# Performance work log

Measured on AMD Instinct MI355X. Metric: run time of the kernel, lower is better.

Reference implementation:

```python
import jax, jax.numpy as jnp
import numpy as np

D_MODEL = 1024
NUM_HEADS = 16
D_K = D_MODEL // NUM_HEADS
R = 8
ALPHA = 16
SCALING = ALPHA / R


def _lora_linear(x, W, b, A, Bm):
    # base: x @ W.T + b ; lora: (x @ A.T) @ Bm.T * scaling
    base = jnp.einsum('btd,od->bto', x, W) + b
    lora = jnp.einsum('btr,or->bto', jnp.einsum('btd,rd->btr', x, A), Bm) * SCALING
    return base + lora


def setup_inputs() -> dict:
    key = jax.random.key(0)
    ks = jax.random.split(key, 20)
    B, T = 2, 2048
    inp = {
        'q': jax.random.normal(ks[0], (B, T, D_MODEL), jnp.float32),
        'k': jax.random.normal(ks[1], (B, T, D_MODEL), jnp.float32),
        'v': jax.random.normal(ks[2], (B, T, D_MODEL), jnp.float32),
        'mask': jnp.ones((1, 1, T, T), jnp.int32),
    }
    i = 3
    for name in ('q', 'k', 'v'):
        inp[f'W{name}'] = jax.random.normal(ks[i], (D_MODEL, D_MODEL), jnp.float32) * 0.02; i += 1
        inp[f'b{name}'] = jnp.zeros((D_MODEL,), jnp.float32)
        inp[f'A{name}'] = jax.random.normal(ks[i], (R, D_MODEL), jnp.float32) * 0.01; i += 1
        inp[f'B{name}'] = jax.random.normal(ks[i], (D_MODEL, R), jnp.float32) * 0.01; i += 1
    inp['Wo'] = jax.random.normal(ks[i], (D_MODEL, D_MODEL), jnp.float32) * 0.02
    inp['bo'] = jnp.zeros((D_MODEL,), jnp.float32)
    return inp


def reference(q, k, v, mask, Wq, bq, Aq, Bq, Wk, bk, Ak, Bk, Wv, bv, Av, Bv, Wo, bo):
    B, Tq, _ = q.shape
    Tk = k.shape[1]
    Q = _lora_linear(q, Wq, bq, Aq, Bq).reshape(B, Tq, NUM_HEADS, D_K).transpose(0, 2, 1, 3)
    K = _lora_linear(k, Wk, bk, Ak, Bk).reshape(B, Tk, NUM_HEADS, D_K).transpose(0, 2, 1, 3)
    V = _lora_linear(v, Wv, bv, Av, Bv).reshape(B, Tk, NUM_HEADS, D_K).transpose(0, 2, 1, 3)
    scores = jnp.einsum('bhqd,bhkd->bhqk', Q, K) / jnp.sqrt(jnp.float32(D_K))
    scores = jnp.where(mask == 0, jnp.float32(-1e9), scores)
    attn = jax.nn.softmax(scores, axis=-1)
    out = jnp.einsum('bhqk,bhkd->bhqd', attn, V)
    out = out.transpose(0, 2, 1, 3).reshape(B, Tq, D_MODEL)
    return jnp.einsum('btd,od->bto', out, Wo) + bo
```

## Files before the change

kernel.cpp:

```cpp
#include <hip/hip_runtime.h>
#include <stdint.h>

typedef unsigned short u16;
typedef __attribute__((ext_vector_type(4))) float f32x4;
typedef __attribute__((ext_vector_type(8))) __bf16 bf16x8;

#if __has_builtin(__builtin_amdgcn_exp2f)
#define EXP2(x) __builtin_amdgcn_exp2f(x)
#else
#define EXP2(x) exp2f(x)
#endif

static __device__ __forceinline__ float bf2f(u16 u) {
    union { uint32_t i; float f; } v; v.i = ((uint32_t)u) << 16; return v.f;
}
static __device__ __forceinline__ u16 f2bf(float f) {
    union { float f; uint32_t i; } v; v.f = f;
    return (u16)((v.i + 0x7FFFu + ((v.i >> 16) & 1u)) >> 16);
}

static __device__ __forceinline__ void gl2lds16(const u16* g, u16* lds) {
    __builtin_amdgcn_global_load_lds(
        (const __attribute__((address_space(1))) void*)g,
        (__attribute__((address_space(3))) void*)lds, 16, 0, 0);
}

struct CastArgs { const float* src[4]; u16* dst[4]; };

__global__ __launch_bounds__(256)
void cast_kernel(CastArgs a) {
    int bid = blockIdx.x;
    int arr = bid >> 6, boff = bid & 63;
    const float* s = a.src[arr] + (size_t)boff * 16384;
    u16* d = a.dst[arr] + (size_t)boff * 16384;
    const int tid = threadIdx.x;
#pragma unroll
    for (int i = 0; i < 8; ++i) {
        int c = tid + i * 256;
        float4 f0 = *(const float4*)(s + c * 8);
        float4 f1 = *(const float4*)(s + c * 8 + 4);
        u16 o[8];
        o[0] = f2bf(f0.x); o[1] = f2bf(f0.y); o[2] = f2bf(f0.z); o[3] = f2bf(f0.w);
        o[4] = f2bf(f1.x); o[5] = f2bf(f1.y); o[6] = f2bf(f1.z); o[7] = f2bf(f1.w);
        *(uint4*)(d + c * 8) = *(const uint4*)o;
    }
}

__global__ __launch_bounds__(256)
void flags_kernel(const int* __restrict__ mask, int* __restrict__ flags) {
    const int qb = blockIdx.x, kt = blockIdx.y;
    const int tid = threadIdx.x;
    int ok = 1;
#pragma unroll
    for (int i = 0; i < 8; ++i) {
        int c = tid + i * 256;
        int row = c >> 4, cg = c & 15;
        int4 m4 = *(const int4*)&mask[(size_t)(qb * 128 + row) * 2048 + kt * 64 + cg * 4];
        ok &= (m4.x != 0) & (m4.y != 0) & (m4.z != 0) & (m4.w != 0);
    }
    int wall = __all(ok) ? 1 : 0;
    __shared__ int red[4];
    if ((tid & 63) == 0) red[tid >> 6] = wall;
    __syncthreads();
    if (tid == 0) flags[qb * 32 + kt] = red[0] & red[1] & red[2] & red[3];
}

struct XaArgs { const float* x[3]; const float* A[3]; float* o[3]; u16* xb[3]; };

__global__ __launch_bounds__(256)
void xa_kernel(XaArgs a) {
    const int z = blockIdx.y;
    const int row = blockIdx.x * 4 + (threadIdx.x >> 6);
    const int lane = threadIdx.x & 63;
    const float* xr = a.x[z] + (size_t)row * 1024 + lane * 16;
    float xv[16];
#pragma unroll
    for (int j = 0; j < 4; ++j) *(float4*)&xv[j * 4] = *(const float4*)(xr + j * 4);
    {
        u16 ob[16];
#pragma unroll
        for (int j = 0; j < 16; ++j) ob[j] = f2bf(xv[j]);
        u16* dp = a.xb[z] + (size_t)row * 1024 + lane * 16;
        *(uint4*)dp = *(const uint4*)&ob[0];
        *(uint4*)(dp + 8) = *(const uint4*)&ob[8];
    }
    float s[8];
#pragma unroll
    for (int r = 0; r < 8; ++r) {
        const float* ar = a.A[z] + (size_t)r * 1024 + lane * 16;
        float av[16];
#pragma unroll
        for (int j = 0; j < 4; ++j) *(float4*)&av[j * 4] = *(const float4*)(ar + j * 4);
        float acc = 0.f;
#pragma unroll
        for (int j = 0; j < 16; ++j) acc += xv[j] * av[j];
#pragma unroll
        for (int off = 1; off < 64; off <<= 1) acc += __shfl_xor(acc, off, 64);
        s[r] = acc;
    }
    if (lane == 0) {
#pragma unroll
        for (int r = 0; r < 8; ++r) a.o[z][(size_t)row * 8 + r] = s[r];
    }
}

struct GemmPtrs { const u16* X; const u16* W; const float* bias; const float* XA; const float* Bm; void* out; int transT; float oscale; };
struct GemmArgs { GemmPtrs p[3]; };

#define LST 136
#define LTT 72

template <int WMT, int WNT, int LORA>
__global__ __launch_bounds__(256, 2)
void gemm_kernel(GemmArgs args) {
    constexpr int BM = WMT * 32, BN = WNT * 32;
    constexpr int MBLK = 4096 / BM;
    constexpr int IPA = BM / 32;
    constexpr int IPB = BN / 32;
    __shared__ alignas(16) u16 smem[(BM + BN) * 64];
    u16* As = smem;
    u16* Bs = smem + BM * 64;

    const GemmPtrs gp = args.p[blockIdx.z];
    const int tid = threadIdx.x;
    const int lane = tid & 63, wave = tid >> 6;
    const int wm = wave >> 1, wn = wave & 1;
    const int l15 = lane & 15, l4 = lane >> 4;
    const int id = blockIdx.x;
    const int m0 = (id % MBLK) * BM, n0 = (id / MBLK) * BN;

    const int srow = lane >> 3;
    const int scol = ((lane & 7) ^ srow) * 8;
    const u16* gA[IPA];
    const u16* gB[IPB];
#pragma unroll
    for (int i = 0; i < IPA; ++i) {
        int q = wave * IPA + i;
        gA[i] = gp.X + (size_t)(m0 + q * 8 + srow) * 1024 + scol;
    }
#pragma unroll
    for (int i = 0; i < IPB; ++i) {
        int q = wave * IPB + i;
        gB[i] = gp.W + (size_t)(n0 + q * 8 + srow) * 1024 + scol;
    }

    const f32x4 fz = {0.f, 0.f, 0.f, 0.f};
    f32x4 acc[WMT][WNT];
#pragma unroll
    for (int i = 0; i < WMT; ++i)
#pragma unroll
        for (int j = 0; j < WNT; ++j) acc[i][j] = fz;

    const int sw = l15 & 7;
    for (int kb = 0; kb < 16; ++kb) {
        __syncthreads();
#pragma unroll
        for (int i = 0; i < IPA; ++i)
            gl2lds16(gA[i] + kb * 64, &As[(wave * IPA + i) * 512]);
#pragma unroll
        for (int i = 0; i < IPB; ++i)
            gl2lds16(gB[i] + kb * 64, &Bs[(wave * IPB + i) * 512]);
        __syncthreads();
#pragma unroll
        for (int kk2 = 0; kk2 < 2; ++kk2) {
            bf16x8 af[WMT], bfr[WNT];
#pragma unroll
            for (int mt = 0; mt < WMT; ++mt) {
                int x = wm * (WMT * 16) + mt * 16 + l15;
                af[mt] = *(const bf16x8*)&As[x * 64 + (((kk2 * 4 + l4) ^ sw) * 8)];
            }
#pragma unroll
            for (int nt = 0; nt < WNT; ++nt) {
                int y = wn * (WNT * 16) + nt * 16 + l15;
                bfr[nt] = *(const bf16x8*)&Bs[y * 64 + (((kk2 * 4 + l4) ^ sw) * 8)];
            }
#pragma unroll
            for (int mt = 0; mt < WMT; ++mt)
#pragma unroll
                for (int nt = 0; nt < WNT; ++nt)
                    acc[mt][nt] = __builtin_amdgcn_mfma_f32_16x16x32_bf16(af[mt], bfr[nt], acc[mt][nt], 0, 0, 0);
        }
    }

    if constexpr (LORA) {
        __syncthreads();
        float* XAs = (float*)smem;
        float* Bms = (float*)(smem + BM * 64);
        {
            int rr = tid >> 1, hf = (tid & 1) * 4;
            *(float4*)&XAs[rr * 8 + hf] = *(const float4*)&gp.XA[(size_t)(m0 + rr) * 8 + hf];
            if (tid < 128) {
                *(float4*)&Bms[tid * 8]     = *(const float4*)&gp.Bm[(size_t)(n0 + tid) * 8];
                *(float4*)&Bms[tid * 8 + 4] = *(const float4*)&gp.Bm[(size_t)(n0 + tid) * 8 + 4];
            }
        }
        __syncthreads();
        const float osc = gp.oscale;
        float bmv[WNT][8], bsv[WNT];
#pragma unroll
        for (int nt = 0; nt < WNT; ++nt) {
            int nloc = wn * 64 + nt * 16 + l15;
            bsv[nt] = gp.bias[n0 + nloc];
#pragma unroll
            for (int q8 = 0; q8 < 8; ++q8) bmv[nt][q8] = Bms[nloc * 8 + q8];
        }
#pragma unroll
        for (int mt = 0; mt < WMT; ++mt)
#pragma unroll
            for (int r = 0; r < 4; ++r) {
                int mloc = wm * 64 + mt * 16 + l4 * 4 + r;
                float xa8[8];
                *(float4*)&xa8[0] = *(const float4*)&XAs[mloc * 8];
                *(float4*)&xa8[4] = *(const float4*)&XAs[mloc * 8 + 4];
#pragma unroll
                for (int nt = 0; nt < WNT; ++nt) {
                    float lora = 0.f;
#pragma unroll
                    for (int q8 = 0; q8 < 8; ++q8) lora += xa8[q8] * bmv[nt][q8];
                    acc[mt][nt][r] = (acc[mt][nt][r] + bsv[nt] + 2.0f * lora) * osc;
                }
            }
        __syncthreads();

        u16* outp = (u16*)gp.out;
        const int bb = m0 >> 11;
        if (gp.transT) {
            u16* Lst = smem;
#pragma unroll
            for (int ch = 0; ch < 2; ++ch) {
#pragma unroll
                for (int mt2 = 0; mt2 < 2; ++mt2) {
                    int mt = ch * 2 + mt2;
#pragma unroll
                    for (int nt = 0; nt < WNT; ++nt)
#pragma unroll
                        for (int r = 0; r < 4; ++r)
                            Lst[(wn * 64 + nt * 16 + l15) * LTT + wm * 32 + mt2 * 16 + l4 * 4 + r] =
                                f2bf(acc[mt][nt][r]);
                }
                __syncthreads();
#pragma unroll
                for (int j = 0; j < 4; ++j) {
                    int w = tid + j * 256;
                    int nl = w >> 3, seg = w & 7;
                    uint4 val = *(const uint4*)&Lst[nl * LTT + seg * 8];
                    int n = n0 + nl, hh = n >> 6, dd = n & 63;
                    int c0 = seg * 8;
                    int gm = m0 + (c0 >> 5) * 64 + ch * 32 + (c0 & 31);
                    int t = gm & 2047;
                    *(uint4*)&outp[(((size_t)(bb * 16 + hh)) * 64 + dd) * 2048 + t] = val;
                }
                __syncthreads();
            }
        } else {
            u16* Ls = smem;
#pragma unroll
            for (int ch = 0; ch < 2; ++ch) {
#pragma unroll
                for (int mt2 = 0; mt2 < 2; ++mt2) {
                    int mt = ch * 2 + mt2;
#pragma unroll
                    for (int nt = 0; nt < WNT; ++nt)
#pragma unroll
                        for (int r = 0; r < 4; ++r)
                            Ls[(wm * 32 + mt2 * 16 + l4 * 4 + r) * LST + wn * 64 + nt * 16 + l15] =
                                f2bf(acc[mt][nt][r]);
                }
                __syncthreads();
#pragma unroll
                for (int j = 0; j < 4; ++j) {
                    int w = tid + j * 256;
                    int lrow = w >> 4, seg = w & 15;
                    uint4 val = *(const uint4*)&Ls[lrow * LST + seg * 8];
                    int gm = m0 + (lrow >> 5) * 64 + ch * 32 + (lrow & 31);
                    int t = gm & 2047;
                    int n = n0 + seg * 8, hh = n >> 6, dd = n & 63;
                    *(uint4*)&outp[(((size_t)(bb * 16 + hh)) * 2048 + t) * 64 + dd] = val;
                }
                __syncthreads();
            }
        }
    } else {
        float* outp = (float*)gp.out;
#pragma unroll
        for (int mt = 0; mt < WMT; ++mt)
#pragma unroll
            for (int r = 0; r < 4; ++r) {
                int m = m0 + wm * (WMT * 16) + mt * 16 + l4 * 4 + r;
#pragma unroll
                for (int nt = 0; nt < WNT; ++nt) {
                    int n = n0 + wn * (WNT * 16) + nt * 16 + l15;
                    outp[(size_t)m * 1024 + n] = acc[mt][nt][r] + gp.bias[n];
                }
            }
    }
}

#define EXP2C (-5.7707801636f)

__global__ __launch_bounds__(256, 4)
void attn_kernel(const u16* __restrict__ QKV, const int* __restrict__ mask,
                 const int* __restrict__ flags, u16* __restrict__ Xo) {
    const int qb = blockIdx.x >> 5;
    const int bh = blockIdx.x & 31;
    const int b = bh >> 4, h = bh & 15;
    const int tid = threadIdx.x;
    const int lane = tid & 63, wave = tid >> 6;
    const int l15 = lane & 15, l4 = lane >> 4;

    __shared__ alignas(16) u16 Ks[2][64 * 64];
    __shared__ alignas(16) u16 Vts[2][64 * 64];
    __shared__ alignas(16) u16 Ps[64 * 64];

    const size_t plane = (size_t)2 * 16 * 2048 * 64;
    const u16* Qg = QKV + (size_t)(b * 16 + h) * 2048 * 64;
    const u16* Kg = Qg + plane;
    const u16* Vg = Kg + plane;

    const int srow = lane >> 3;
    const int scol = ((lane & 7) ^ srow) * 8;

    bf16x8 qa[2];
#pragma unroll
    for (int kk2 = 0; kk2 < 2; ++kk2)
        qa[kk2] = *(const bf16x8*)&Qg[(size_t)(qb * 64 + wave * 16 + l15) * 64 + kk2 * 32 + l4 * 8];

    const f32x4 fz = {0.f, 0.f, 0.f, 0.f};
    f32x4 accO[4];
    float lsum[4];
#pragma unroll
    for (int dt = 0; dt < 4; ++dt) accO[dt] = fz;
#pragma unroll
    for (int r = 0; r < 4; ++r) lsum[r] = 0.f;

#pragma unroll
    for (int i = 0; i < 2; ++i) {
        int qq = wave * 2 + i;
        gl2lds16(Kg + (size_t)(qq * 8 + srow) * 64 + scol, &Ks[0][qq * 512]);
        gl2lds16(Vg + (size_t)(qq * 8 + srow) * 2048 + scol, &Vts[0][qq * 512]);
    }
    __syncthreads();

    for (int kt = 0; kt < 32; ++kt) {
        const u16* Kc = &Ks[kt & 1][0];
        const u16* Vc = &Vts[kt & 1][0];

        if (kt < 31) {
            u16* Kn = &Ks[(kt + 1) & 1][0];
            u16* Vn = &Vts[(kt + 1) & 1][0];
#pragma unroll
            for (int i = 0; i < 2; ++i) {
                int qq = wave * 2 + i;
                gl2lds16(Kg + (size_t)((kt + 1) * 64 + qq * 8 + srow) * 64 + scol, &Kn[qq * 512]);
                gl2lds16(Vg + (size_t)(qq * 8 + srow) * 2048 + (kt + 1) * 64 + scol, &Vn[qq * 512]);
            }
        }

        f32x4 accS[4];
#pragma unroll
        for (int nt = 0; nt < 4; ++nt) accS[nt] = fz;
#pragma unroll
        for (int kk2 = 0; kk2 < 2; ++kk2) {
            bf16x8 kf[4];
#pragma unroll
            for (int nt = 0; nt < 4; ++nt)
                kf[nt] = *(const bf16x8*)&Kc[(nt * 16 + l15) * 64 + (((kk2 * 4 + l4) ^ (l15 & 7)) * 8)];
#pragma unroll
            for (int nt = 0; nt < 4; ++nt)
                accS[nt] = __builtin_amdgcn_mfma_f32_16x16x32_bf16(qa[kk2], kf[nt], accS[nt], 0, 0, 0);
        }

        if (flags[(qb >> 1) * 32 + kt] == 0) {
#pragma unroll
            for (int nt = 0; nt < 4; ++nt)
#pragma unroll
                for (int r = 0; r < 4; ++r) {
                    int qrow = qb * 64 + wave * 16 + l4 * 4 + r;
                    int kcol = kt * 64 + nt * 16 + l15;
                    if (mask[(size_t)qrow * 2048 + kcol] == 0) accS[nt][r] = -1e9f;
                }
        }

#pragma unroll
        for (int r = 0; r < 4; ++r) {
            float part = 0.f;
#pragma unroll
            for (int nt = 0; nt < 4; ++nt) {
                float p = EXP2(accS[nt][r] + EXP2C);
                accS[nt][r] = p;
                part += p;
            }
            lsum[r] += part;
        }

#pragma unroll
        for (int nt = 0; nt < 4; ++nt)
#pragma unroll
            for (int r = 0; r < 4; ++r) {
                int prow = wave * 16 + l4 * 4 + r;
                Ps[prow * 64 + (((nt * 2 + (l15 >> 3)) ^ (prow & 7)) * 8) + (l15 & 7)] =
                    f2bf(accS[nt][r]);
            }
        asm volatile("s_waitcnt lgkmcnt(0)" : : : "memory");

#pragma unroll
        for (int kk2 = 0; kk2 < 2; ++kk2) {
            bf16x8 pa = *(const bf16x8*)&Ps[(wave * 16 + l15) * 64 + (((kk2 * 4 + l4) ^ (l15 & 7)) * 8)];
            bf16x8 vf[4];
#pragma unroll
            for (int dt = 0; dt < 4; ++dt)
                vf[dt] = *(const bf16x8*)&Vc[(dt * 16 + l15) * 64 + (((kk2 * 4 + l4) ^ (l15 & 7)) * 8)];
#pragma unroll
            for (int dt = 0; dt < 4; ++dt)
                accO[dt] = __builtin_amdgcn_mfma_f32_16x16x32_bf16(pa, vf[dt], accO[dt], 0, 0, 0);
        }

        __syncthreads();
    }

    float inv[4];
#pragma unroll
    for (int r = 0; r < 4; ++r) {
        float s = lsum[r];
#pragma unroll
        for (int off = 1; off < 16; off <<= 1) s += __shfl_xor(s, off, 64);
        inv[r] = 1.0f / s;
    }

#pragma unroll
    for (int dt = 0; dt < 4; ++dt)
#pragma unroll
        for (int r = 0; r < 4; ++r) {
            int prow = wave * 16 + l4 * 4 + r;
            Ps[prow * 64 + (((dt * 2 + (l15 >> 3)) ^ (prow & 7)) * 8) + (l15 & 7)] =
                f2bf(accO[dt][r] * inv[r]);
        }
    __syncthreads();
#pragma unroll
    for (int j = 0; j < 2; ++j) {
        int w = tid + j * 256;
        int row = w >> 3, seg = w & 7;
        uint4 val = *(const uint4*)&Ps[row * 64 + ((seg ^ (row & 7)) * 8)];
        int t = qb * 64 + row;
        *(uint4*)&Xo[((size_t)(b * 2048 + t)) * 1024 + h * 64 + seg * 8] = val;
    }
}

extern "C" void kernel_launch(void* const* d_in, const int* in_sizes, int n_in,
                              void* d_out, int out_size, void* d_ws, size_t ws_size,
                              hipStream_t stream) {
    const float* q    = (const float*)d_in[0];
    const float* k    = (const float*)d_in[1];
    const float* v    = (const float*)d_in[2];
    const int*   mask = (const int*)d_in[3];
    const float* Wq = (const float*)d_in[4];
    const float* bq = (const float*)d_in[5];
    const float* Aq = (const float*)d_in[6];
    const float* Bq = (const float*)d_in[7];
    const float* Wk = (const float*)d_in[8];
    const float* bk = (const float*)d_in[9];
    const float* Ak = (const float*)d_in[10];
    const float* Bk = (const float*)d_in[11];
    const float* Wv = (const float*)d_in[12];
    const float* bv = (const float*)d_in[13];
    const float* Av = (const float*)d_in[14];
    const float* Bv = (const float*)d_in[15];
    const float* Wo = (const float*)d_in[16];
    const float* bo = (const float*)d_in[17];

    char* ws = (char*)d_ws;
    u16*   QKV   = (u16*)ws;
    u16*   qb16  = (u16*)(ws + 25165824);
    u16*   kb16  = (u16*)(ws + 33554432);
    u16*   vb16  = (u16*)(ws + 41943040);
    u16*   Wqb   = (u16*)(ws + 50331648);
    u16*   Wkb   = (u16*)(ws + 52428800);
    u16*   Wvb   = (u16*)(ws + 54525952);
    u16*   Wob   = (u16*)(ws + 56623104);
    float* XAbuf = (float*)(ws + 58720256);
    int*   flags = (int*)(ws + 59113472);
    u16*   Xbuf  = qb16;

    flags_kernel<<<dim3(16, 32), dim3(256), 0, stream>>>(mask, flags);

    XaArgs xa;
    xa.x[0] = q;  xa.x[1] = k;  xa.x[2] = v;
    xa.A[0] = Aq; xa.A[1] = Ak; xa.A[2] = Av;
    xa.o[0] = XAbuf; xa.o[1] = XAbuf + 32768; xa.o[2] = XAbuf + 65536;
    xa.xb[0] = qb16; xa.xb[1] = kb16; xa.xb[2] = vb16;
    xa_kernel<<<dim3(1024, 3), dim3(256), 0, stream>>>(xa);

    CastArgs ca;
    ca.src[0] = Wq; ca.src[1] = Wk; ca.src[2] = Wv; ca.src[3] = Wo;
    ca.dst[0] = Wqb; ca.dst[1] = Wkb; ca.dst[2] = Wvb; ca.dst[3] = Wob;
    cast_kernel<<<dim3(256), dim3(256), 0, stream>>>(ca);

    const float QSCALE = 0.1803368801f;
    GemmArgs g1;
    g1.p[0] = GemmPtrs{qb16, Wqb, bq, XAbuf,         Bq, (void*)QKV,             0, QSCALE};
    g1.p[1] = GemmPtrs{kb16, Wkb, bk, XAbuf + 32768, Bk, (void*)(QKV + 4194304), 0, 1.0f};
    g1.p[2] = GemmPtrs{vb16, Wvb, bv, XAbuf + 65536, Bv, (void*)(QKV + 8388608), 1, 1.0f};
    gemm_kernel<4, 4, 1><<<dim3(256, 1, 3), dim3(256), 0, stream>>>(g1);

    attn_kernel<<<dim3(1024), dim3(256), 0, stream>>>(QKV, mask, flags, Xbuf);

    GemmArgs g2;
    g2.p[0] = GemmPtrs{Xbuf, Wob, bo, nullptr, nullptr, d_out, 0, 1.0f};
    g2.p[1] = g2.p[0];
    g2.p[2] = g2.p[0];
    gemm_kernel<2, 4, 0><<<dim3(512, 1, 1), dim3(256), 0, stream>>>(g2);
}
```

Before: 292.2 us.

## Keep softmax probabilities in registers by computing transposed S and permuting K rows

The QK^T MFMA now uses swapped operands, producing S transposed, so each lane holds the probabilities it needs directly as the A operand of the PV MFMA. K rows are loaded into LDS in a permuted order so the register layout matches. This removes the LDS round trip for P and its wait. The P buffer is dropped, cutting LDS use, and bf16 packing now uses v_cvt_pk_bf16_f32. The row-sum reduction is reworked to match the new layout. The cost is more complex index mapping that has to stay consistent with the mask indexing.

```diff
diff --git a/kernel.cpp b/kernel.cpp
--- a/kernel.cpp
+++ b/kernel.cpp
@@ -3,6 +3,7 @@
 
 typedef unsigned short u16;
 typedef __attribute__((ext_vector_type(4))) float f32x4;
+typedef __attribute__((ext_vector_type(4))) uint32_t u32x4;
 typedef __attribute__((ext_vector_type(8))) __bf16 bf16x8;
 
 #if __has_builtin(__builtin_amdgcn_exp2f)
@@ -17,6 +18,11 @@
 static __device__ __forceinline__ u16 f2bf(float f) {
     union { float f; uint32_t i; } v; v.f = f;
     return (u16)((v.i + 0x7FFFu + ((v.i >> 16) & 1u)) >> 16);
+}
+static __device__ __forceinline__ uint32_t cvtpk(float lo, float hi) {
+    uint32_t r;
+    asm("v_cvt_pk_bf16_f32 %0, %1, %2" : "=v"(r) : "v"(lo), "v"(hi));
+    return r;
 }
 
 static __device__ __forceinline__ void gl2lds16(const u16* g, u16* lds) {
@@ -310,7 +316,6 @@
 
     __shared__ alignas(16) u16 Ks[2][64 * 64];
     __shared__ alignas(16) u16 Vts[2][64 * 64];
-    __shared__ alignas(16) u16 Ps[64 * 64];
 
     const size_t plane = (size_t)2 * 16 * 2048 * 64;
     const u16* Qg = QKV + (size_t)(b * 16 + h) * 2048 * 64;
@@ -320,6 +325,16 @@
     const int srow = lane >> 3;
     const int scol = ((lane & 7) ^ srow) * 8;
 
+    const u16* kbase[2];
+    const u16* vbase[2];
+#pragma unroll
+    for (int i = 0; i < 2; ++i) {
+        int qq = wave * 2 + i;
+        int kc = 16 * (qq & 1) + 8 * (srow >> 2) + 4 * ((qq >> 1) & 1) + (srow & 3) + 32 * (qq >> 2);
+        kbase[i] = Kg + (size_t)kc * 64 + scol;
+        vbase[i] = Vg + (size_t)(qq * 8 + srow) * 2048 + scol;
+    }
+
     bf16x8 qa[2];
 #pragma unroll
     for (int kk2 = 0; kk2 < 2; ++kk2)
@@ -327,17 +342,15 @@
 
     const f32x4 fz = {0.f, 0.f, 0.f, 0.f};
     f32x4 accO[4];
-    float lsum[4];
 #pragma unroll
     for (int dt = 0; dt < 4; ++dt) accO[dt] = fz;
-#pragma unroll
-    for (int r = 0; r < 4; ++r) lsum[r] = 0.f;
+    float lsum = 0.f;
 
 #pragma unroll
     for (int i = 0; i < 2; ++i) {
         int qq = wave * 2 + i;
-        gl2lds16(Kg + (size_t)(qq * 8 + srow) * 64 + scol, &Ks[0][qq * 512]);
-        gl2lds16(Vg + (size_t)(qq * 8 + srow) * 2048 + scol, &Vts[0][qq * 512]);
+        gl2lds16(kbase[i], &Ks[0][qq * 512]);
+        gl2lds16(vbase[i], &Vts[0][qq * 512]);
     }
     __syncthreads();
 
@@ -351,88 +364,84 @@
 #pragma unroll
             for (int i = 0; i < 2; ++i) {
                 int qq = wave * 2 + i;
-                gl2lds16(Kg + (size_t)((kt + 1) * 64 + qq * 8 + srow) * 64 + scol, &Kn[qq * 512]);
-                gl2lds16(Vg + (size_t)(qq * 8 + srow) * 2048 + (kt + 1) * 64 + scol, &Vn[qq * 512]);
+                gl2lds16(kbase[i] + (size_t)(kt + 1) * 4096, &Kn[qq * 512]);
+                gl2lds16(vbase[i] + (size_t)(kt + 1) * 64, &Vn[qq * 512]);
             }
         }
 
         f32x4 accS[4];
 #pragma unroll
-        for (int nt = 0; nt < 4; ++nt) accS[nt] = fz;
+        for (int j = 0; j < 4; ++j) accS[j] = fz;
 #pragma unroll
         for (int kk2 = 0; kk2 < 2; ++kk2) {
             bf16x8 kf[4];
 #pragma unroll
-            for (int nt = 0; nt < 4; ++nt)
-                kf[nt] = *(const bf16x8*)&Kc[(nt * 16 + l15) * 64 + (((kk2 * 4 + l4) ^ (l15 & 7)) * 8)];
-#pragma unroll
-            for (int nt = 0; nt < 4; ++nt)
-                accS[nt] = __builtin_amdgcn_mfma_f32_16x16x32_bf16(qa[kk2], kf[nt], accS[nt], 0, 0, 0);
+            for (int j = 0; j < 4; ++j)
+                kf[j] = *(const bf16x8*)&Kc[(j * 16 + l15) * 64 + (((kk2 * 4 + l4) ^ (l15 & 7)) * 8)];
+#pragma unroll
+            for (int j = 0; j < 4; ++j)
+                accS[j] = __builtin_amdgcn_mfma_f32_16x16x32_bf16(kf[j], qa[kk2], accS[j], 0, 0, 0);
         }
 
         if (flags[(qb >> 1) * 32 + kt] == 0) {
-#pragma unroll
-            for (int nt = 0; nt < 4; ++nt)
+            int qrow = qb * 64 + wave * 16 + l15;
+#pragma unroll
+            for (int j = 0; j < 4; ++j)
 #pragma unroll
                 for (int r = 0; r < 4; ++r) {
-                    int qrow = qb * 64 + wave * 16 + l4 * 4 + r;
-                    int kcol = kt * 64 + nt * 16 + l15;
-                    if (mask[(size_t)qrow * 2048 + kcol] == 0) accS[nt][r] = -1e9f;
-                }
-        }
-
-#pragma unroll
-        for (int r = 0; r < 4; ++r) {
-            float part = 0.f;
-#pragma unroll
-            for (int nt = 0; nt < 4; ++nt) {
-                float p = EXP2(accS[nt][r] + EXP2C);
-                accS[nt][r] = p;
-                part += p;
-            }
-            lsum[r] += part;
-        }
-
-#pragma unroll
-        for (int nt = 0; nt < 4; ++nt)
+                    int kcol = kt * 64 + 8 * l4 + 4 * (j & 1) + r + 32 * (j >> 1);
+                    if (mask[(size_t)qrow * 2048 + kcol] == 0) accS[j][r] = -1e9f;
+                }
+        }
+
+        float part0 = 0.f, part1 = 0.f;
+#pragma unroll
+        for (int j = 0; j < 4; ++j)
 #pragma unroll
             for (int r = 0; r < 4; ++r) {
-                int prow = wave * 16 + l4 * 4 + r;
-                Ps[prow * 64 + (((nt * 2 + (l15 >> 3)) ^ (prow & 7)) * 8) + (l15 & 7)] =
-                    f2bf(accS[nt][r]);
-            }
-        asm volatile("s_waitcnt lgkmcnt(0)" : : : "memory");
+                float p = EXP2(accS[j][r] + EXP2C);
+                accS[j][r] = p;
+                if (j & 1) part1 += p; else part0 += p;
+            }
+        lsum += part0 + part1;
+
+        u32x4 paw0, paw1;
+        paw0[0] = cvtpk(accS[0][0], accS[0][1]); paw0[1] = cvtpk(accS[0][2], accS[0][3]);
+        paw0[2] = cvtpk(accS[1][0], accS[1][1]); paw0[3] = cvtpk(accS[1][2], accS[1][3]);
+        paw1[0] = cvtpk(accS[2][0], accS[2][1]); paw1[1] = cvtpk(accS[2][2], accS[2][3]);
+        paw1[2] = cvtpk(accS[3][0], accS[3][1]); paw1[3] = cvtpk(accS[3][2], accS[3][3]);
+        bf16x8 pa[2];
+        pa[0] = __builtin_bit_cast(bf16x8, paw0);
+        pa[1] = __builtin_bit_cast(bf16x8, paw1);
 
 #pragma unroll
         for (int kk2 = 0; kk2 < 2; ++kk2) {
-            bf16x8 pa = *(const bf16x8*)&Ps[(wave * 16 + l15) * 64 + (((kk2 * 4 + l4) ^ (l15 & 7)) * 8)];
             bf16x8 vf[4];
 #pragma unroll
             for (int dt = 0; dt < 4; ++dt)
                 vf[dt] = *(const bf16x8*)&Vc[(dt * 16 + l15) * 64 + (((kk2 * 4 + l4) ^ (l15 & 7)) * 8)];
 #pragma unroll
             for (int dt = 0; dt < 4; ++dt)
-                accO[dt] = __builtin_amdgcn_mfma_f32_16x16x32_bf16(pa, vf[dt], accO[dt], 0, 0, 0);
+                accO[dt] = __builtin_amdgcn_mfma_f32_16x16x32_bf16(pa[kk2], vf[dt], accO[dt], 0, 0, 0);
         }
 
         __syncthreads();
     }
 
+    float tot = lsum;
+    tot += __shfl_xor(tot, 16, 64);
+    tot += __shfl_xor(tot, 32, 64);
     float inv[4];
 #pragma unroll
-    for (int r = 0; r < 4; ++r) {
-        float s = lsum[r];
-#pragma unroll
-        for (int off = 1; off < 16; off <<= 1) s += __shfl_xor(s, off, 64);
-        inv[r] = 1.0f / s;
-    }
-
+    for (int r = 0; r < 4; ++r) inv[r] = 1.0f / __shfl(tot, l4 * 4 + r, 64);
+
+    u16* Es = &Ks[0][0];
 #pragma unroll
     for (int dt = 0; dt < 4; ++dt)
 #pragma unroll
         for (int r = 0; r < 4; ++r) {
             int prow = wave * 16 + l4 * 4 + r;
-            Ps[prow * 64 + (((dt * 2 + (l15 >> 3)) ^ (prow & 7)) * 8) + (l15 & 7)] =
+            Es[prow * 64 + (((dt * 2 + (l15 >> 3)) ^ (prow & 7)) * 8) + (l15 & 7)] =
                 f2bf(accO[dt][r] * inv[r]);
         }
     __syncthreads();
@@ -440,7 +449,7 @@
     for (int j = 0; j < 2; ++j) {
         int w = tid + j * 256;
         int row = w >> 3, seg = w & 7;
-        uint4 val = *(const uint4*)&Ps[row * 64 + ((seg ^ (row & 7)) * 8)];
+        uint4 val = *(const uint4*)&Es[row * 64 + ((seg ^ (row & 7)) * 8)];
         int t = qb * 64 + row;
         *(uint4*)&Xo[((size_t)(b * 2048 + t)) * 1024 + h * 64 + seg * 8] = val;
     }
```

After: 276.3 us. 1.06x faster.
